# Kernel tuning notes

Hardware: AMD Instinct MI355X
Metric: run time of the kernel (lower is better)

## Reference

```python
import jax, jax.numpy as jnp
import numpy as np

N_ATOMS = 100000
N_EDGES = 1600000
N_FRAGS = 10000
N_FRAG_EDGES = 80000
D = 128


def setup_inputs() -> dict:
    key = jax.random.key(0)
    ks = jax.random.split(key, 16)
    s = 1.0 / np.sqrt(D)
    return {
        "x_atoms": jax.random.normal(ks[0], (N_ATOMS, D), jnp.float32),
        "edge_index": jax.random.randint(ks[1], (2, N_EDGES), 0, N_ATOMS),
        "edge_attr": jax.random.normal(ks[2], (N_EDGES, D), jnp.float32),
        "frag_index": jax.random.randint(ks[3], (2, N_FRAG_EDGES), 0, N_FRAGS),
        "x_frags": jax.random.normal(ks[4], (N_FRAGS, D), jnp.float32),
        "atom_to_frag_ids": jax.random.randint(ks[5], (N_ATOMS,), 0, N_FRAGS),
        # parameters (stored [in, out]); only layers actually used in forward
        "atom_w": jax.random.uniform(ks[6], (D, D), jnp.float32, -s, s),
        "atom_b": jax.random.uniform(ks[7], (D,), jnp.float32, -s, s),
        "edge_w": jax.random.uniform(ks[8], (D, D), jnp.float32, -s, s),
        "edge_b": jax.random.uniform(ks[9], (D,), jnp.float32, -s, s),
        "frag_w1": jax.random.uniform(ks[10], (D, 2 * D), jnp.float32, -s, s),
        "frag_b1": jax.random.uniform(ks[11], (2 * D,), jnp.float32, -s, s),
        "frag_w2": jax.random.uniform(ks[12], (2 * D, D), jnp.float32, -(1.0 / np.sqrt(2 * D)), 1.0 / np.sqrt(2 * D)),
        "frag_b2": jax.random.uniform(ks[13], (D,), jnp.float32, -(1.0 / np.sqrt(2 * D)), 1.0 / np.sqrt(2 * D)),
    }


def reference(x_atoms, edge_index, edge_attr, frag_index, x_frags,
              atom_to_frag_ids, atom_w, atom_b, edge_w, edge_b,
              frag_w1, frag_b1, frag_w2, frag_b2):
    n = x_atoms.shape[0]
    n_frags = x_frags.shape[0]

    # add self loops
    loop = jnp.arange(n, dtype=edge_index.dtype)
    src = jnp.concatenate([edge_index[0], loop])
    tgt = jnp.concatenate([edge_index[1], loop])
    self_loop_attr = jnp.zeros((n, edge_attr.shape[1]), edge_attr.dtype)
    edge_attr_full = jnp.concatenate([edge_attr, self_loop_attr], axis=0)

    # embeddings
    h = x_atoms @ atom_w + atom_b                      # [N, D]
    _e = edge_attr_full @ edge_w + edge_b              # computed but unused (as in source)

    # symmetric degree normalization over source-node degree
    deg = jax.ops.segment_sum(jnp.ones_like(src, dtype=h.dtype), src, num_segments=n)
    dinv = jnp.where(deg > 0, deg ** -0.5, 0.0)
    norm = dinv[src] * dinv[tgt]                       # [E+N]

    # gather - scale - scatter_add
    msg = h[src] * norm[:, None]                       # [E+N, D]
    x_atoms_new = jax.ops.segment_sum(msg, tgt, num_segments=n)

    # pool atoms into fragments
    frag_feats = jax.ops.segment_sum(x_atoms_new, atom_to_frag_ids, num_segments=n_frags)

    # fragment-level message passing
    fsrc, ftgt = frag_index[0], frag_index[1]
    frag_sum = jax.ops.segment_sum(frag_feats[fsrc], ftgt, num_segments=n_frags)

    # frag_mlp: Linear(D, 2D) -> ReLU -> Linear(2D, D)
    x_frags_new = jax.nn.relu(frag_sum @ frag_w1 + frag_b1) @ frag_w2 + frag_b2
    return (x_atoms_new, x_frags_new)
```

## Files before the change

kernel.cpp:

```cpp
#include <hip/hip_runtime.h>

constexpr int DD = 128;

typedef __attribute__((ext_vector_type(8))) short short8_t;
typedef __attribute__((ext_vector_type(4))) float f32x4;

__device__ __forceinline__ float bf2f(unsigned short u) {
  union { unsigned int i; float f; } c;
  c.i = ((unsigned int)u) << 16;
  return c.f;
}
__device__ __forceinline__ unsigned short f2bf(float f) {
  union { float f; unsigned int i; } c;
  c.f = f;
  unsigned int x = c.i;
  x += 0x7fff + ((x >> 16) & 1);
  return (unsigned short)(x >> 16);
}

__global__ void __launch_bounds__(256) mfma_h_k(
    const float* __restrict__ x, const float* __restrict__ W,
    const float* __restrict__ bias, const float* __restrict__ dinv,
    unsigned short* __restrict__ out, int nrows) {
  __shared__ unsigned int wt[8192];

  const int tid = threadIdx.x;
  const int rbase = blockIdx.x * 128;

  {
    int c = tid & 127;
    int half = tid >> 7;
#pragma unroll 4
    for (int j = 0; j < 32; j++) {
      int p = j * 2 + half;
      int k = p * 2;
      float w0 = W[k * 128 + c];
      float w1 = W[(k + 1) * 128 + c];
      unsigned int packed = (unsigned int)f2bf(w0) | ((unsigned int)f2bf(w1) << 16);
      wt[(64 * c + p) ^ ((c & 7) << 2)] = packed;
    }
  }

  const int wave = tid >> 6;
  const int lane = tid & 63;
  const int l15 = lane & 15;
  const int kg = lane >> 4;

  float bcol[8];
#pragma unroll
  for (int ct = 0; ct < 8; ct++) bcol[ct] = bias[ct * 16 + l15];
  float dv[8];
#pragma unroll
  for (int rt = 0; rt < 2; rt++)
#pragma unroll
    for (int i = 0; i < 4; i++) {
      int gr = rbase + wave * 32 + rt * 16 + kg * 4 + i;
      dv[rt * 4 + i] = (gr < nrows) ? dinv[gr] : 0.f;
    }

  __syncthreads();

  f32x4 acc[2][8];
#pragma unroll
  for (int rt = 0; rt < 2; rt++)
#pragma unroll
    for (int ct = 0; ct < 8; ct++) acc[rt][ct] = (f32x4)(0.f);

#pragma unroll
  for (int ks = 0; ks < 4; ks++) {
    int kcol = ks * 32 + kg * 8;
    short8_t a[2];
#pragma unroll
    for (int rt = 0; rt < 2; rt++) {
      int row = rbase + wave * 32 + rt * 16 + l15;
      if (row < nrows) {
        const float4* xr = reinterpret_cast<const float4*>(x + (size_t)row * 128 + kcol);
        float4 v0 = xr[0], v1 = xr[1];
        a[rt][0] = (short)f2bf(v0.x); a[rt][1] = (short)f2bf(v0.y);
        a[rt][2] = (short)f2bf(v0.z); a[rt][3] = (short)f2bf(v0.w);
        a[rt][4] = (short)f2bf(v1.x); a[rt][5] = (short)f2bf(v1.y);
        a[rt][6] = (short)f2bf(v1.z); a[rt][7] = (short)f2bf(v1.w);
      } else {
#pragma unroll
        for (int e = 0; e < 8; e++) a[rt][e] = 0;
      }
    }
#pragma unroll
    for (int ct = 0; ct < 8; ct++) {
      int col = ct * 16 + l15;
      int dw0 = (64 * col + ks * 16 + kg * 4) ^ ((col & 7) << 2);
      short8_t b = *reinterpret_cast<const short8_t*>(&wt[dw0]);
      acc[0][ct] = __builtin_amdgcn_mfma_f32_16x16x32_bf16(a[0], b, acc[0][ct], 0, 0, 0);
      acc[1][ct] = __builtin_amdgcn_mfma_f32_16x16x32_bf16(a[1], b, acc[1][ct], 0, 0, 0);
    }
  }

#pragma unroll
  for (int rt = 0; rt < 2; rt++)
#pragma unroll
    for (int ct = 0; ct < 8; ct++)
#pragma unroll
      for (int i = 0; i < 4; i++) {
        int gr = rbase + wave * 32 + rt * 16 + kg * 4 + i;
        if (gr < nrows)
          out[(size_t)gr * 128 + ct * 16 + l15] =
              f2bf((acc[rt][ct][i] + bcol[ct]) * dv[rt * 4 + i]);
      }
}

template<int IC, int OC, bool RELU, int RPT>
__global__ void __launch_bounds__(256) linear_k(
    const float* __restrict__ in, const float* __restrict__ W,
    const float* __restrict__ bias, float* __restrict__ out, int nrows) {
  constexpr int GROUPS = 256 / OC;
  constexpr int RBLK = RPT * GROUPS;
  __shared__ float xs[RBLK * IC];
  const int tid = threadIdx.x;
  const int c = tid % OC;
  const int g = tid / OC;
  const int rbase = blockIdx.x * RBLK;

  constexpr int NV = RBLK * IC / 4;
  const float4* in4 = reinterpret_cast<const float4*>(in);
  for (int idx = tid; idx < NV; idx += 256) {
    int r = idx / (IC / 4);
    int kk = idx % (IC / 4);
    int gr = rbase + r;
    float4 v = make_float4(0.f, 0.f, 0.f, 0.f);
    if (gr < nrows) v = in4[(size_t)gr * (IC / 4) + kk];
    reinterpret_cast<float4*>(xs)[idx] = v;
  }
  __syncthreads();

  float acc[RPT];
  float b = bias[c];
#pragma unroll
  for (int m = 0; m < RPT; m++) acc[m] = b;

#pragma unroll 4
  for (int k = 0; k < IC; k++) {
    float w = W[k * OC + c];
#pragma unroll
    for (int m = 0; m < RPT; m++)
      acc[m] += xs[(g + m * GROUPS) * IC + k] * w;
  }

#pragma unroll
  for (int m = 0; m < RPT; m++) {
    int gr = rbase + g + m * GROUPS;
    if (gr < nrows) {
      float v = acc[m];
      if (RELU) v = fmaxf(v, 0.f);
      out[(size_t)gr * OC + c] = v;
    }
  }
}

__global__ void __launch_bounds__(256) counts_k(
    const int* __restrict__ esrc, const int* __restrict__ etgt, int E,
    const int* __restrict__ a2f, int N,
    const int* __restrict__ ftgt, int FE,
    int* __restrict__ cnt_src, int* __restrict__ cnt_tgt,
    int* __restrict__ cnt_a2f, int* __restrict__ cnt_fe,
    int* __restrict__ rank_tgt, int* __restrict__ rank_a2f,
    int* __restrict__ rank_fe) {
  int i = blockIdx.x * 256 + threadIdx.x;
  if (i < E) {
    atomicAdd(&cnt_src[esrc[i]], 1);
    rank_tgt[i] = atomicAdd(&cnt_tgt[etgt[i]], 1);
  } else if (i < E + N) {
    int j = i - E;
    rank_a2f[j] = atomicAdd(&cnt_a2f[a2f[j]], 1);
  } else if (i < E + N + FE) {
    int e = i - E - N;
    rank_fe[e] = atomicAdd(&cnt_fe[ftgt[e]], 1);
  }
}

constexpr int SCAN_C = 1024;

__global__ void __launch_bounds__(256) scan_bsum_k(const int* __restrict__ in, int n,
                                                   int* __restrict__ bsums) {
  __shared__ int s[256];
  int t = threadIdx.x;
  int base = blockIdx.x * SCAN_C;
  int v = 0;
  for (int i = t; i < SCAN_C; i += 256) {
    int g = base + i;
    if (g < n) v += in[g];
  }
  s[t] = v;
  __syncthreads();
  for (int d = 128; d > 0; d >>= 1) {
    if (t < d) s[t] += s[t + d];
    __syncthreads();
  }
  if (t == 0) bsums[blockIdx.x] = s[0];
}

__global__ void __launch_bounds__(1024) scan_small_k(int* __restrict__ bsums, int nb) {
  __shared__ int s[1024];
  int t = threadIdx.x;
  int v = (t < nb) ? bsums[t] : 0;
  s[t] = v;
  __syncthreads();
  for (int d = 1; d < 1024; d <<= 1) {
    int u = (t >= d) ? s[t - d] : 0;
    __syncthreads();
    s[t] += u;
    __syncthreads();
  }
  if (t < nb) bsums[t] = s[t] - v;
}

__global__ void __launch_bounds__(256) scan_final_dinv_k(
    const int* __restrict__ in, int n, const int* __restrict__ bsums,
    int* __restrict__ off, const int* __restrict__ cnt_src,
    float* __restrict__ dinv) {
  __shared__ int s[256];
  int t = threadIdx.x;
  int base = blockIdx.x * SCAN_C + t * 4;
  int a0 = (base + 0 < n) ? in[base + 0] : 0;
  int a1 = (base + 1 < n) ? in[base + 1] : 0;
  int a2 = (base + 2 < n) ? in[base + 2] : 0;
  int a3 = (base + 3 < n) ? in[base + 3] : 0;
  int tot = a0 + a1 + a2 + a3;
  s[t] = tot;
  __syncthreads();
  for (int d = 1; d < 256; d <<= 1) {
    int u = (t >= d) ? s[t - d] : 0;
    __syncthreads();
    s[t] += u;
    __syncthreads();
  }
  int pre = s[t] - tot + bsums[blockIdx.x];
  int e0 = pre, e1 = pre + a0, e2 = e1 + a1, e3 = e2 + a2;
  if (base + 0 < n) { off[base + 0] = e0; dinv[base + 0] = rsqrtf((float)(cnt_src[base + 0] + 1)); }
  if (base + 1 < n) { off[base + 1] = e1; dinv[base + 1] = rsqrtf((float)(cnt_src[base + 1] + 1)); }
  if (base + 2 < n) { off[base + 2] = e2; dinv[base + 2] = rsqrtf((float)(cnt_src[base + 2] + 1)); }
  if (base + 3 < n) { off[base + 3] = e3; dinv[base + 3] = rsqrtf((float)(cnt_src[base + 3] + 1)); }
}

__global__ void __launch_bounds__(1024) scan2_k(
    const int* __restrict__ in0, int n0, int* __restrict__ off0,
    const int* __restrict__ in1, int n1, int* __restrict__ off1) {
  __shared__ int s[1024];
  const int* in = blockIdx.x == 0 ? in0 : in1;
  int n = blockIdx.x == 0 ? n0 : n1;
  int* off = blockIdx.x == 0 ? off0 : off1;
  int t = threadIdx.x;
  int carry = 0;
  for (int base = 0; base < n; base += 1024) {
    int v = (base + t < n) ? in[base + t] : 0;
    __syncthreads();
    s[t] = v;
    __syncthreads();
    for (int d = 1; d < 1024; d <<= 1) {
      int u = (t >= d) ? s[t - d] : 0;
      __syncthreads();
      s[t] += u;
      __syncthreads();
    }
    int tot = s[1023];
    if (base + t < n) off[base + t] = s[t] - v + carry;
    carry += tot;
  }
}

__global__ void __launch_bounds__(256) fill_k(
    const int* __restrict__ esrc, const int* __restrict__ etgt, int E,
    const int* __restrict__ a2f, int N,
    const int* __restrict__ fsrc, const int* __restrict__ ftgt, int FE,
    const int* __restrict__ off_tgt, const int* __restrict__ rank_tgt,
    const int* __restrict__ off_a2f, const int* __restrict__ rank_a2f,
    const int* __restrict__ off_fe, const int* __restrict__ rank_fe,
    int* __restrict__ csr_src, int* __restrict__ aids, int* __restrict__ csr_fs) {
  int i = blockIdx.x * 256 + threadIdx.x;
  if (i < E) {
    csr_src[off_tgt[etgt[i]] + rank_tgt[i]] = esrc[i];
  } else if (i < E + N) {
    int j = i - E;
    aids[off_a2f[a2f[j]] + rank_a2f[j]] = j;
  } else if (i < E + N + FE) {
    int e = i - E - N;
    csr_fs[off_fe[ftgt[e]] + rank_fe[e]] = fsrc[e];
  }
}

__global__ void __launch_bounds__(256) edge_gather_k(
    const int* __restrict__ off, const int* __restrict__ cnt,
    const int* __restrict__ csr_src, const unsigned short* __restrict__ h,
    const float* __restrict__ dinv, float* __restrict__ out, int n) {
  int tn = blockIdx.x * 8 + (threadIdx.x >> 5);
  if (tn >= n) return;
  int lane = threadIdx.x & 31;
  const ushort4* h4 = reinterpret_cast<const ushort4*>(h);
  ushort4 hv = h4[(size_t)tn * 32 + lane];
  float ax = bf2f(hv.x), ay = bf2f(hv.y), az = bf2f(hv.z), aw = bf2f(hv.w);
  int s0 = off[tn], c = cnt[tn];
  int i = 0;
  for (; i + 4 <= c; i += 4) {
    int s1 = csr_src[s0 + i + 0];
    int s2 = csr_src[s0 + i + 1];
    int s3 = csr_src[s0 + i + 2];
    int s4 = csr_src[s0 + i + 3];
    ushort4 v1 = h4[(size_t)s1 * 32 + lane];
    ushort4 v2 = h4[(size_t)s2 * 32 + lane];
    ushort4 v3 = h4[(size_t)s3 * 32 + lane];
    ushort4 v4 = h4[(size_t)s4 * 32 + lane];
    ax += (bf2f(v1.x) + bf2f(v2.x)) + (bf2f(v3.x) + bf2f(v4.x));
    ay += (bf2f(v1.y) + bf2f(v2.y)) + (bf2f(v3.y) + bf2f(v4.y));
    az += (bf2f(v1.z) + bf2f(v2.z)) + (bf2f(v3.z) + bf2f(v4.z));
    aw += (bf2f(v1.w) + bf2f(v2.w)) + (bf2f(v3.w) + bf2f(v4.w));
  }
  for (; i < c; i++) {
    int s1 = csr_src[s0 + i];
    ushort4 v1 = h4[(size_t)s1 * 32 + lane];
    ax += bf2f(v1.x); ay += bf2f(v1.y); az += bf2f(v1.z); aw += bf2f(v1.w);
  }
  float dt = dinv[tn];
  reinterpret_cast<float4*>(out)[(size_t)tn * 32 + lane] =
      make_float4(ax * dt, ay * dt, az * dt, aw * dt);
}

__global__ void __launch_bounds__(256) seg_gather_k(
    const int* __restrict__ off, const int* __restrict__ cnt,
    const int* __restrict__ ids, const float* __restrict__ src_rows,
    float* __restrict__ dst, int n) {
  int f = blockIdx.x * 8 + (threadIdx.x >> 5);
  if (f >= n) return;
  int lane = threadIdx.x & 31;
  const float4* s4 = reinterpret_cast<const float4*>(src_rows);
  float ax = 0.f, ay = 0.f, az = 0.f, aw = 0.f;
  int s0 = off[f], c = cnt[f];
  int i = 0;
  for (; i + 2 <= c; i += 2) {
    int a1 = ids[s0 + i], a2 = ids[s0 + i + 1];
    float4 v1 = s4[(size_t)a1 * 32 + lane];
    float4 v2 = s4[(size_t)a2 * 32 + lane];
    ax += v1.x + v2.x; ay += v1.y + v2.y; az += v1.z + v2.z; aw += v1.w + v2.w;
  }
  if (i < c) {
    int a1 = ids[s0 + i];
    float4 v1 = s4[(size_t)a1 * 32 + lane];
    ax += v1.x; ay += v1.y; az += v1.z; aw += v1.w;
  }
  reinterpret_cast<float4*>(dst)[(size_t)f * 32 + lane] = make_float4(ax, ay, az, aw);
}

extern "C" void kernel_launch(void* const* d_in, const int* in_sizes, int n_in,
                              void* d_out, int out_size, void* d_ws, size_t ws_size,
                              hipStream_t stream) {
  const float* x_atoms    = (const float*)d_in[0];
  const int*   edge_index = (const int*)d_in[1];
  const int*   frag_index = (const int*)d_in[3];
  const int*   a2f     = (const int*)d_in[5];
  const float* atom_w  = (const float*)d_in[6];
  const float* atom_b  = (const float*)d_in[7];
  const float* frag_w1 = (const float*)d_in[10];
  const float* frag_b1 = (const float*)d_in[11];
  const float* frag_w2 = (const float*)d_in[12];
  const float* frag_b2 = (const float*)d_in[13];

  const int N  = in_sizes[0] / DD;
  const int E  = in_sizes[1] / 2;
  const int FE = in_sizes[3] / 2;
  const int NF = in_sizes[4] / DD;

  const int* esrc = edge_index;
  const int* etgt = edge_index + E;
  const int* fsrc = frag_index;
  const int* ftgt = frag_index + FE;

  float* out_atoms = (float*)d_out;
  float* out_frags = out_atoms + (size_t)N * DD;

  char* ws = (char*)d_ws;
  size_t off_b = 0;
  auto alloc = [&](size_t bytes) {
    void* p = ws + off_b;
    off_b += (bytes + 255) & ~(size_t)255;
    return p;
  };
  unsigned short* h = (unsigned short*)alloc((size_t)N * DD * 2);
  float* dinv     = (float*)alloc((size_t)N * 4);
  int*   cnts     = (int*)alloc(((size_t)2 * N + 2 * NF) * 4);
  int*   cnt_src  = cnts;
  int*   cnt_tgt  = cnts + N;
  int*   cnt_a2f  = cnts + 2 * N;
  int*   cnt_fe   = cnts + 2 * N + NF;
  int*   off_tgt  = (int*)alloc((size_t)N * 4);
  int*   rank_tgt = (int*)alloc((size_t)E * 4);
  int*   csr_src  = (int*)alloc((size_t)E * 4);
  int*   off_a2f  = (int*)alloc((size_t)NF * 4);
  int*   rank_a2f = (int*)alloc((size_t)N * 4);
  int*   aids     = (int*)alloc((size_t)N * 4);
  int*   off_fe   = (int*)alloc((size_t)NF * 4);
  int*   rank_fe  = (int*)alloc((size_t)FE * 4);
  int*   csr_fs   = (int*)alloc((size_t)FE * 4);
  int*   bsums    = (int*)alloc(1024 * 4);
  float* ff       = (float*)alloc((size_t)NF * DD * 4);
  float* fs       = (float*)alloc((size_t)NF * DD * 4);
  float* hid      = (float*)alloc((size_t)NF * 2 * DD * 4);

  hipMemsetAsync(cnts, 0, ((size_t)2 * N + 2 * NF) * 4, stream);

  counts_k<<<(E + N + FE + 255) / 256, 256, 0, stream>>>(
      esrc, etgt, E, a2f, N, ftgt, FE,
      cnt_src, cnt_tgt, cnt_a2f, cnt_fe, rank_tgt, rank_a2f, rank_fe);

  int nb1 = (N + SCAN_C - 1) / SCAN_C;
  scan_bsum_k<<<nb1, 256, 0, stream>>>(cnt_tgt, N, bsums);
  scan_small_k<<<1, 1024, 0, stream>>>(bsums, nb1);
  scan_final_dinv_k<<<nb1, 256, 0, stream>>>(cnt_tgt, N, bsums, off_tgt, cnt_src, dinv);
  scan2_k<<<2, 1024, 0, stream>>>(cnt_a2f, NF, off_a2f, cnt_fe, NF, off_fe);

  fill_k<<<(E + N + FE + 255) / 256, 256, 0, stream>>>(
      esrc, etgt, E, a2f, N, fsrc, ftgt, FE,
      off_tgt, rank_tgt, off_a2f, rank_a2f, off_fe, rank_fe,
      csr_src, aids, csr_fs);

  mfma_h_k<<<(N + 127) / 128, 256, 0, stream>>>(x_atoms, atom_w, atom_b, dinv, h, N);

  edge_gather_k<<<(N + 7) / 8, 256, 0, stream>>>(off_tgt, cnt_tgt, csr_src, h, dinv, out_atoms, N);
  seg_gather_k<<<(NF + 7) / 8, 256, 0, stream>>>(off_a2f, cnt_a2f, aids, out_atoms, ff, NF);
  seg_gather_k<<<(NF + 7) / 8, 256, 0, stream>>>(off_fe, cnt_fe, csr_fs, ff, fs, NF);

  linear_k<128, 256, true, 32><<<(NF + 31) / 32, 256, 0, stream>>>(fs, frag_w1, frag_b1, hid, NF);
  linear_k<256, 128, false, 16><<<(NF + 31) / 32, 256, 0, stream>>>(hid, frag_w2, frag_b2, out_frags, NF);
}
```

Baseline: 396.9 us.

## Fuse counting into GEMM launch, merge scans, widen edge gather lanes

The atom-embedding GEMM no longer depends on dinv. It is launched in the same grid as the atomic degree counting, so the two independent jobs overlap and one launch goes away. The dinv scaling of source rows moves into the edge gather, which now reads dinv per neighbour. The scan kernels are merged from four launches into two, with a per-block recomputed prefix replacing the single-block scan. The edge gather uses 16 lanes per node with 8-element bf16 loads. The cost is extra dinv lookups per edge and redundant prefix sums in each scan block.

```diff
diff --git a/kernel.cpp b/kernel.cpp
--- a/kernel.cpp
+++ b/kernel.cpp
@@ -3,6 +3,7 @@
 constexpr int DD = 128;
 
 typedef __attribute__((ext_vector_type(8))) short short8_t;
+typedef __attribute__((ext_vector_type(8))) unsigned short ushort8_t;
 typedef __attribute__((ext_vector_type(4))) float f32x4;
 
 __device__ __forceinline__ float bf2f(unsigned short u) {
@@ -18,11 +19,31 @@
   return (unsigned short)(x >> 16);
 }
 
-__global__ void __launch_bounds__(256) mfma_h_k(
+__global__ void __launch_bounds__(256) counts_gemm_k(
+    const int* __restrict__ esrc, const int* __restrict__ etgt, int E,
+    const int* __restrict__ a2f, int N, const int* __restrict__ ftgt, int FE,
+    int* __restrict__ cnt_src, int* __restrict__ cnt_tgt,
+    int* __restrict__ cnt_a2f, int* __restrict__ cnt_fe,
+    int* __restrict__ rank_tgt, int* __restrict__ rank_a2f, int* __restrict__ rank_fe,
     const float* __restrict__ x, const float* __restrict__ W,
-    const float* __restrict__ bias, const float* __restrict__ dinv,
-    unsigned short* __restrict__ out, int nrows) {
+    const float* __restrict__ bias, unsigned short* __restrict__ hout,
+    int nb_gemm) {
   __shared__ unsigned int wt[8192];
+
+  if ((int)blockIdx.x >= nb_gemm) {
+    int i = ((int)blockIdx.x - nb_gemm) * 256 + threadIdx.x;
+    if (i < E) {
+      atomicAdd(&cnt_src[esrc[i]], 1);
+      rank_tgt[i] = atomicAdd(&cnt_tgt[etgt[i]], 1);
+    } else if (i < E + N) {
+      int j = i - E;
+      rank_a2f[j] = atomicAdd(&cnt_a2f[a2f[j]], 1);
+    } else if (i < E + N + FE) {
+      int e = i - E - N;
+      rank_fe[e] = atomicAdd(&cnt_fe[ftgt[e]], 1);
+    }
+    return;
+  }
 
   const int tid = threadIdx.x;
   const int rbase = blockIdx.x * 128;
@@ -49,14 +70,6 @@
   float bcol[8];
 #pragma unroll
   for (int ct = 0; ct < 8; ct++) bcol[ct] = bias[ct * 16 + l15];
-  float dv[8];
-#pragma unroll
-  for (int rt = 0; rt < 2; rt++)
-#pragma unroll
-    for (int i = 0; i < 4; i++) {
-      int gr = rbase + wave * 32 + rt * 16 + kg * 4 + i;
-      dv[rt * 4 + i] = (gr < nrows) ? dinv[gr] : 0.f;
-    }
 
   __syncthreads();
 
@@ -73,7 +86,7 @@
 #pragma unroll
     for (int rt = 0; rt < 2; rt++) {
       int row = rbase + wave * 32 + rt * 16 + l15;
-      if (row < nrows) {
+      if (row < N) {
         const float4* xr = reinterpret_cast<const float4*>(x + (size_t)row * 128 + kcol);
         float4 v0 = xr[0], v1 = xr[1];
         a[rt][0] = (short)f2bf(v0.x); a[rt][1] = (short)f2bf(v0.y);
@@ -102,9 +115,8 @@
 #pragma unroll
       for (int i = 0; i < 4; i++) {
         int gr = rbase + wave * 32 + rt * 16 + kg * 4 + i;
-        if (gr < nrows)
-          out[(size_t)gr * 128 + ct * 16 + l15] =
-              f2bf((acc[rt][ct][i] + bcol[ct]) * dv[rt * 4 + i]);
+        if (gr < N)
+          hout[(size_t)gr * 128 + ct * 16 + l15] = f2bf(acc[rt][ct][i] + bcol[ct]);
       }
 }
 
@@ -156,70 +168,65 @@
   }
 }
 
-__global__ void __launch_bounds__(256) counts_k(
-    const int* __restrict__ esrc, const int* __restrict__ etgt, int E,
-    const int* __restrict__ a2f, int N,
-    const int* __restrict__ ftgt, int FE,
-    int* __restrict__ cnt_src, int* __restrict__ cnt_tgt,
-    int* __restrict__ cnt_a2f, int* __restrict__ cnt_fe,
-    int* __restrict__ rank_tgt, int* __restrict__ rank_a2f,
-    int* __restrict__ rank_fe) {
-  int i = blockIdx.x * 256 + threadIdx.x;
-  if (i < E) {
-    atomicAdd(&cnt_src[esrc[i]], 1);
-    rank_tgt[i] = atomicAdd(&cnt_tgt[etgt[i]], 1);
-  } else if (i < E + N) {
-    int j = i - E;
-    rank_a2f[j] = atomicAdd(&cnt_a2f[a2f[j]], 1);
-  } else if (i < E + N + FE) {
-    int e = i - E - N;
-    rank_fe[e] = atomicAdd(&cnt_fe[ftgt[e]], 1);
-  }
-}
-
-constexpr int SCAN_C = 1024;
-
-__global__ void __launch_bounds__(256) scan_bsum_k(const int* __restrict__ in, int n,
-                                                   int* __restrict__ bsums) {
+__global__ void __launch_bounds__(256) scanA_k(
+    const int* __restrict__ cnt_tgt, int n, int nb, int* __restrict__ bsums,
+    const int* __restrict__ cnt_a2f, int* __restrict__ off_a2f,
+    const int* __restrict__ cnt_fe, int* __restrict__ off_fe, int nf) {
   __shared__ int s[256];
   int t = threadIdx.x;
-  int base = blockIdx.x * SCAN_C;
-  int v = 0;
-  for (int i = t; i < SCAN_C; i += 256) {
-    int g = base + i;
-    if (g < n) v += in[g];
-  }
-  s[t] = v;
-  __syncthreads();
-  for (int d = 128; d > 0; d >>= 1) {
-    if (t < d) s[t] += s[t + d];
+  int bid = blockIdx.x;
+  if (bid < nb) {
+    int base = bid * 1024;
+    int v = 0;
+    for (int i = t; i < 1024; i += 256) {
+      int g = base + i;
+      if (g < n) v += cnt_tgt[g];
+    }
+    s[t] = v;
     __syncthreads();
-  }
-  if (t == 0) bsums[blockIdx.x] = s[0];
-}
-
-__global__ void __launch_bounds__(1024) scan_small_k(int* __restrict__ bsums, int nb) {
-  __shared__ int s[1024];
-  int t = threadIdx.x;
-  int v = (t < nb) ? bsums[t] : 0;
-  s[t] = v;
-  __syncthreads();
-  for (int d = 1; d < 1024; d <<= 1) {
-    int u = (t >= d) ? s[t - d] : 0;
-    __syncthreads();
-    s[t] += u;
-    __syncthreads();
-  }
-  if (t < nb) bsums[t] = s[t] - v;
-}
-
-__global__ void __launch_bounds__(256) scan_final_dinv_k(
+    for (int d = 128; d > 0; d >>= 1) {
+      if (t < d) s[t] += s[t + d];
+      __syncthreads();
+    }
+    if (t == 0) bsums[bid] = s[0];
+  } else {
+    const int* in = (bid == nb) ? cnt_a2f : cnt_fe;
+    int* off = (bid == nb) ? off_a2f : off_fe;
+    int carry = 0;
+    for (int base = 0; base < nf; base += 256) {
+      int v = (base + t < nf) ? in[base + t] : 0;
+      __syncthreads();
+      s[t] = v;
+      __syncthreads();
+      for (int d = 1; d < 256; d <<= 1) {
+        int u = (t >= d) ? s[t - d] : 0;
+        __syncthreads();
+        s[t] += u;
+        __syncthreads();
+      }
+      if (base + t < nf) off[base + t] = s[t] - v + carry;
+      carry += s[255];
+    }
+  }
+}
+
+__global__ void __launch_bounds__(256) scanB_k(
     const int* __restrict__ in, int n, const int* __restrict__ bsums,
     int* __restrict__ off, const int* __restrict__ cnt_src,
     float* __restrict__ dinv) {
   __shared__ int s[256];
   int t = threadIdx.x;
-  int base = blockIdx.x * SCAN_C + t * 4;
+  int bid = blockIdx.x;
+  s[t] = (t < bid) ? bsums[t] : 0;
+  __syncthreads();
+  for (int d = 128; d > 0; d >>= 1) {
+    if (t < d) s[t] += s[t + d];
+    __syncthreads();
+  }
+  int prefix = s[0];
+  __syncthreads();
+
+  int base = bid * 1024 + t * 4;
   int a0 = (base + 0 < n) ? in[base + 0] : 0;
   int a1 = (base + 1 < n) ? in[base + 1] : 0;
   int a2 = (base + 2 < n) ? in[base + 2] : 0;
@@ -233,38 +240,12 @@
     s[t] += u;
     __syncthreads();
   }
-  int pre = s[t] - tot + bsums[blockIdx.x];
+  int pre = s[t] - tot + prefix;
   int e0 = pre, e1 = pre + a0, e2 = e1 + a1, e3 = e2 + a2;
   if (base + 0 < n) { off[base + 0] = e0; dinv[base + 0] = rsqrtf((float)(cnt_src[base + 0] + 1)); }
   if (base + 1 < n) { off[base + 1] = e1; dinv[base + 1] = rsqrtf((float)(cnt_src[base + 1] + 1)); }
   if (base + 2 < n) { off[base + 2] = e2; dinv[base + 2] = rsqrtf((float)(cnt_src[base + 2] + 1)); }
   if (base + 3 < n) { off[base + 3] = e3; dinv[base + 3] = rsqrtf((float)(cnt_src[base + 3] + 1)); }
-}
-
-__global__ void __launch_bounds__(1024) scan2_k(
-    const int* __restrict__ in0, int n0, int* __restrict__ off0,
-    const int* __restrict__ in1, int n1, int* __restrict__ off1) {
-  __shared__ int s[1024];
-  const int* in = blockIdx.x == 0 ? in0 : in1;
-  int n = blockIdx.x == 0 ? n0 : n1;
-  int* off = blockIdx.x == 0 ? off0 : off1;
-  int t = threadIdx.x;
-  int carry = 0;
-  for (int base = 0; base < n; base += 1024) {
-    int v = (base + t < n) ? in[base + t] : 0;
-    __syncthreads();
-    s[t] = v;
-    __syncthreads();
-    for (int d = 1; d < 1024; d <<= 1) {
-      int u = (t >= d) ? s[t - d] : 0;
-      __syncthreads();
-      s[t] += u;
-      __syncthreads();
-    }
-    int tot = s[1023];
-    if (base + t < n) off[base + t] = s[t] - v + carry;
-    carry += tot;
-  }
 }
 
 __global__ void __launch_bounds__(256) fill_k(
@@ -291,12 +272,15 @@
     const int* __restrict__ off, const int* __restrict__ cnt,
     const int* __restrict__ csr_src, const unsigned short* __restrict__ h,
     const float* __restrict__ dinv, float* __restrict__ out, int n) {
-  int tn = blockIdx.x * 8 + (threadIdx.x >> 5);
+  int tn = blockIdx.x * 16 + (threadIdx.x >> 4);
   if (tn >= n) return;
-  int lane = threadIdx.x & 31;
-  const ushort4* h4 = reinterpret_cast<const ushort4*>(h);
-  ushort4 hv = h4[(size_t)tn * 32 + lane];
-  float ax = bf2f(hv.x), ay = bf2f(hv.y), az = bf2f(hv.z), aw = bf2f(hv.w);
+  int lane = threadIdx.x & 15;
+  const ushort8_t* h8 = reinterpret_cast<const ushort8_t*>(h);
+  float dt = dinv[tn];
+  ushort8_t hv = h8[(size_t)tn * 16 + lane];
+  float acc[8];
+#pragma unroll
+  for (int e = 0; e < 8; e++) acc[e] = bf2f(hv[e]) * dt;
   int s0 = off[tn], c = cnt[tn];
   int i = 0;
   for (; i + 4 <= c; i += 4) {
@@ -304,23 +288,26 @@
     int s2 = csr_src[s0 + i + 1];
     int s3 = csr_src[s0 + i + 2];
     int s4 = csr_src[s0 + i + 3];
-    ushort4 v1 = h4[(size_t)s1 * 32 + lane];
-    ushort4 v2 = h4[(size_t)s2 * 32 + lane];
-    ushort4 v3 = h4[(size_t)s3 * 32 + lane];
-    ushort4 v4 = h4[(size_t)s4 * 32 + lane];
-    ax += (bf2f(v1.x) + bf2f(v2.x)) + (bf2f(v3.x) + bf2f(v4.x));
-    ay += (bf2f(v1.y) + bf2f(v2.y)) + (bf2f(v3.y) + bf2f(v4.y));
-    az += (bf2f(v1.z) + bf2f(v2.z)) + (bf2f(v3.z) + bf2f(v4.z));
-    aw += (bf2f(v1.w) + bf2f(v2.w)) + (bf2f(v3.w) + bf2f(v4.w));
+    float d1 = dinv[s1], d2 = dinv[s2], d3 = dinv[s3], d4 = dinv[s4];
+    ushort8_t v1 = h8[(size_t)s1 * 16 + lane];
+    ushort8_t v2 = h8[(size_t)s2 * 16 + lane];
+    ushort8_t v3 = h8[(size_t)s3 * 16 + lane];
+    ushort8_t v4 = h8[(size_t)s4 * 16 + lane];
+#pragma unroll
+    for (int e = 0; e < 8; e++)
+      acc[e] += (bf2f(v1[e]) * d1 + bf2f(v2[e]) * d2) +
+                (bf2f(v3[e]) * d3 + bf2f(v4[e]) * d4);
   }
   for (; i < c; i++) {
     int s1 = csr_src[s0 + i];
-    ushort4 v1 = h4[(size_t)s1 * 32 + lane];
-    ax += bf2f(v1.x); ay += bf2f(v1.y); az += bf2f(v1.z); aw += bf2f(v1.w);
-  }
-  float dt = dinv[tn];
-  reinterpret_cast<float4*>(out)[(size_t)tn * 32 + lane] =
-      make_float4(ax * dt, ay * dt, az * dt, aw * dt);
+    float d1 = dinv[s1];
+    ushort8_t v1 = h8[(size_t)s1 * 16 + lane];
+#pragma unroll
+    for (int e = 0; e < 8; e++) acc[e] += bf2f(v1[e]) * d1;
+  }
+  float4* o4 = reinterpret_cast<float4*>(out) + (size_t)tn * 32 + lane * 2;
+  o4[0] = make_float4(acc[0] * dt, acc[1] * dt, acc[2] * dt, acc[3] * dt);
+  o4[1] = make_float4(acc[4] * dt, acc[5] * dt, acc[6] * dt, acc[7] * dt);
 }
 
 __global__ void __launch_bounds__(256) seg_gather_k(
@@ -405,24 +392,24 @@
 
   hipMemsetAsync(cnts, 0, ((size_t)2 * N + 2 * NF) * 4, stream);
 
-  counts_k<<<(E + N + FE + 255) / 256, 256, 0, stream>>>(
+  int nb_gemm = (N + 127) / 128;
+  int nb_cnt = (E + N + FE + 255) / 256;
+  counts_gemm_k<<<nb_gemm + nb_cnt, 256, 0, stream>>>(
       esrc, etgt, E, a2f, N, ftgt, FE,
-      cnt_src, cnt_tgt, cnt_a2f, cnt_fe, rank_tgt, rank_a2f, rank_fe);
-
-  int nb1 = (N + SCAN_C - 1) / SCAN_C;
-  scan_bsum_k<<<nb1, 256, 0, stream>>>(cnt_tgt, N, bsums);
-  scan_small_k<<<1, 1024, 0, stream>>>(bsums, nb1);
-  scan_final_dinv_k<<<nb1, 256, 0, stream>>>(cnt_tgt, N, bsums, off_tgt, cnt_src, dinv);
-  scan2_k<<<2, 1024, 0, stream>>>(cnt_a2f, NF, off_a2f, cnt_fe, NF, off_fe);
-
-  fill_k<<<(E + N + FE + 255) / 256, 256, 0, stream>>>(
+      cnt_src, cnt_tgt, cnt_a2f, cnt_fe, rank_tgt, rank_a2f, rank_fe,
+      x_atoms, atom_w, atom_b, h, nb_gemm);
+
+  int nb1 = (N + 1023) / 1024;
+  scanA_k<<<nb1 + 2, 256, 0, stream>>>(cnt_tgt, N, nb1, bsums,
+                                       cnt_a2f, off_a2f, cnt_fe, off_fe, NF);
+  scanB_k<<<nb1, 256, 0, stream>>>(cnt_tgt, N, bsums, off_tgt, cnt_src, dinv);
+
+  fill_k<<<nb_cnt, 256, 0, stream>>>(
       esrc, etgt, E, a2f, N, fsrc, ftgt, FE,
       off_tgt, rank_tgt, off_a2f, rank_a2f, off_fe, rank_fe,
       csr_src, aids, csr_fs);
 
-  mfma_h_k<<<(N + 127) / 128, 256, 0, stream>>>(x_atoms, atom_w, atom_b, dinv, h, N);
-
-  edge_gather_k<<<(N + 7) / 8, 256, 0, stream>>>(off_tgt, cnt_tgt, csr_src, h, dinv, out_atoms, N);
+  edge_gather_k<<<(N + 15) / 16, 256, 0, stream>>>(off_tgt, cnt_tgt, csr_src, h, dinv, out_atoms, N);
   seg_gather_k<<<(NF + 7) / 8, 256, 0, stream>>>(off_a2f, cnt_a2f, aids, out_atoms, ff, NF);
   seg_gather_k<<<(NF + 7) / 8, 256, 0, stream>>>(off_fe, cnt_fe, csr_fs, ff, fs, NF);
 
```

After: 397.5 us. About the same (+0.1%).
